# Kernel tuning notes

Hardware: AMD Instinct MI355X
Metric: run time of the kernel (lower is better)

Reference implementation:

```python
import jax, jax.numpy as jnp
import numpy as np

NUM_HEADS = 16
HEAD_DIM = 64  # hidden = 1024


def setup_inputs() -> dict:
    key = jax.random.key(0)
    k1, k2, k3 = jax.random.split(key, 3)
    B, S, Hd = 4, 4096, NUM_HEADS * HEAD_DIM
    x = jax.random.normal(k1, (B, S, Hd), dtype=jnp.float32)
    # xavier-uniform-ish scaling for the dense kernels
    Wqkv = jax.random.normal(k2, (Hd, 3 * Hd), dtype=jnp.float32) * (2.0 / (Hd + 3 * Hd)) ** 0.5
    bqkv = jnp.zeros((3 * Hd,), dtype=jnp.float32)
    Wout = jax.random.normal(k3, (Hd, Hd), dtype=jnp.float32) * (1.0 / Hd) ** 0.5
    bout = jnp.zeros((Hd,), dtype=jnp.float32)
    return {"x": x, "Wqkv": Wqkv, "bqkv": bqkv, "Wout": Wout, "bout": bout}


def reference(x, Wqkv, bqkv, Wout, bout):
    B, S, _ = x.shape
    H, D = NUM_HEADS, HEAD_DIM
    qkv = jnp.einsum('bsc,cf->bsf', x, Wqkv) + bqkv  # [B,S,3*H*D]
    q, k, v = jnp.split(qkv, 3, axis=-1)
    # source transposes to [B,H,S,D] before calling flax dot_product_attention_weights,
    # which interprets dims as [..., q_len=H, num_heads=S, depth=D]  (shape bug, kept faithfully)
    q = q.reshape(B, S, H, D).transpose(0, 2, 1, 3)  # [B,H,S,D]
    k = k.reshape(B, S, H, D).transpose(0, 2, 1, 3)
    v = v.reshape(B, S, H, D).transpose(0, 2, 1, 3)
    scale = D ** -0.5
    # flax: einsum('...qhd,...khd->...hqk') -> weights [B, S, H, H]
    logits = jnp.einsum('bqhd,bkhd->bhqk', q * scale, k)
    attn = jax.nn.softmax(logits, axis=-1)  # softmax over key-head axis
    # source: einsum('bhqk,bkhd->bqhd', weights, v) -> [B, H, S, D]
    out = jnp.einsum('bhqk,bkhd->bqhd', attn, v)
    out = out.transpose(0, 2, 1, 3).reshape(B, S, H * D)  # [B,S,hidden]
    return jnp.einsum('bsc,cf->bsf', out, Wout) + bout
```

## Files before the change

kernel.cpp:

```cpp
#include <hip/hip_runtime.h>
#include <hip/hip_bf16.h>

using bf16 = __hip_bfloat16;
typedef __bf16 bf16x8_t __attribute__((ext_vector_type(8)));
typedef float f32x4_t __attribute__((ext_vector_type(4)));

__device__ __forceinline__ void gl16(bf16* l, const bf16* g) {
  __builtin_amdgcn_global_load_lds(
      (const __attribute__((address_space(1))) unsigned int*)g,
      (__attribute__((address_space(3))) unsigned int*)l, 16, 0, 0);
}

__global__ __launch_bounds__(256) void cvt_f32_bf16(const float* __restrict__ in,
                                                    bf16* __restrict__ out, int n4) {
  int i = blockIdx.x * 256 + threadIdx.x;
  if (i >= n4) return;
  float4 v = ((const float4*)in)[i];
  union { ushort4 u; bf16 b[4]; } o;
  o.b[0] = __float2bfloat16(v.x);
  o.b[1] = __float2bfloat16(v.y);
  o.b[2] = __float2bfloat16(v.z);
  o.b[3] = __float2bfloat16(v.w);
  ((ushort4*)out)[i] = o.u;
}

__global__ __launch_bounds__(256) void transpose_cvt(const float* __restrict__ in,
                                                     bf16* __restrict__ out, int R, int C) {
  __shared__ float t[32][33];
  int bx = blockIdx.x * 32, by = blockIdx.y * 32;
  int tx = threadIdx.x & 31, ty = threadIdx.x >> 5;
#pragma unroll
  for (int r = 0; r < 32; r += 8)
    t[ty + r][tx] = in[(size_t)(by + ty + r) * C + bx + tx];
  __syncthreads();
#pragma unroll
  for (int r = 0; r < 32; r += 8)
    out[(size_t)(bx + ty + r) * R + by + tx] = __float2bfloat16(t[tx][ty + r]);
}

template <int OUT_BF16>
__global__ __launch_bounds__(256, 2) void gemm_bt(const bf16* __restrict__ A,
                                                  const bf16* __restrict__ Bt,
                                                  const float* __restrict__ bias,
                                                  void* __restrict__ Cv,
                                                  int M, int N, int K) {
  __shared__ __align__(16) bf16 As[128 * 32];
  __shared__ __align__(16) bf16 Bs[128 * 32];
  const int tid = threadIdx.x;
  const int m0 = blockIdx.y * 128, n0 = blockIdx.x * 128;
  const int w = tid >> 6, lane = tid & 63;
  const int wr = w >> 1, wc = w & 1;
  const int lr = lane & 15, lk = (lane >> 4) << 3;

  const int srow = tid >> 2;
  const int scol = (tid & 3) << 3;
  const bf16* ga0 = A + (size_t)(m0 + srow) * K + scol;
  const bf16* ga1 = A + (size_t)(m0 + srow + 64) * K + scol;
  const bf16* gb0 = Bt + (size_t)(n0 + srow) * K + scol;
  const bf16* gb1 = Bt + (size_t)(n0 + srow + 64) * K + scol;
  bf16* la0 = As + tid * 8;
  bf16* la1 = As + (tid + 256) * 8;
  bf16* lb0 = Bs + tid * 8;
  bf16* lb1 = Bs + (tid + 256) * 8;

  f32x4_t acc[4][4] = {};

  for (int k0 = 0; k0 < K; k0 += 32) {
    gl16(la0, ga0); gl16(la1, ga1);
    gl16(lb0, gb0); gl16(lb1, gb1);
    ga0 += 32; ga1 += 32; gb0 += 32; gb1 += 32;
    __syncthreads();

    bf16x8_t af[4], bfv[4];
#pragma unroll
    for (int m = 0; m < 4; ++m)
      af[m] = *(const bf16x8_t*)(As + ((wr * 64 + m * 16 + lr) * 32 + lk));
#pragma unroll
    for (int n = 0; n < 4; ++n)
      bfv[n] = *(const bf16x8_t*)(Bs + ((wc * 64 + n * 16 + lr) * 32 + lk));
#pragma unroll
    for (int m = 0; m < 4; ++m)
#pragma unroll
      for (int n = 0; n < 4; ++n)
        acc[m][n] = __builtin_amdgcn_mfma_f32_16x16x32_bf16(af[m], bfv[n], acc[m][n], 0, 0, 0);
    __syncthreads();
  }

  const int r0 = (lane >> 4) << 2;
#pragma unroll
  for (int m = 0; m < 4; ++m) {
    int row = m0 + wr * 64 + m * 16 + r0;
#pragma unroll
    for (int n = 0; n < 4; ++n) {
      int col = n0 + wc * 64 + n * 16 + lr;
      float bv = bias[col];
#pragma unroll
      for (int j = 0; j < 4; ++j) {
        float v = acc[m][n][j] + bv;
        if (OUT_BF16)
          ((bf16*)Cv)[(size_t)(row + j) * N + col] = __float2bfloat16(v);
        else
          ((float*)Cv)[(size_t)(row + j) * N + col] = v;
      }
    }
  }
}

#define PSTR 48
__global__ __launch_bounds__(256) void attn_tok(const bf16* __restrict__ qkv,
                                                bf16* __restrict__ out) {
  __shared__ __align__(16) bf16 vs[4][1024];
  __shared__ __align__(16) bf16 ps[4][16 * PSTR];
  const int w = threadIdx.x >> 6, l = threadIdx.x & 63;
  const int t = blockIdx.x * 4 + w;
  const int lr = l & 15, lg = l >> 4;
  const bf16* base = qkv + (size_t)t * 3072;

  bf16x8_t v0 = *(const bf16x8_t*)(base + 2048 + l * 16);
  bf16x8_t v1 = *(const bf16x8_t*)(base + 2048 + l * 16 + 8);
  *(bf16x8_t*)(&vs[w][l * 16]) = v0;
  *(bf16x8_t*)(&vs[w][l * 16 + 8]) = v1;

  *(unsigned long long*)(&ps[w][(l >> 2) * PSTR + 16 + (l & 3) * 4]) = 0ULL;

  const bf16* qp = base + lr * 64 + lg * 8;
  const bf16* kp = base + 1024 + lr * 64 + lg * 8;
  bf16x8_t qa0 = *(const bf16x8_t*)qp;
  bf16x8_t ka0 = *(const bf16x8_t*)kp;
  bf16x8_t qa1 = *(const bf16x8_t*)(qp + 32);
  bf16x8_t ka1 = *(const bf16x8_t*)(kp + 32);
  f32x4_t s = {};
  s = __builtin_amdgcn_mfma_f32_16x16x32_bf16(qa0, ka0, s, 0, 0, 0);
  s = __builtin_amdgcn_mfma_f32_16x16x32_bf16(qa1, ka1, s, 0, 0, 0);

#pragma unroll
  for (int j = 0; j < 4; ++j) {
    float x = s[j] * 0.125f;
    float mx = x;
#pragma unroll
    for (int off = 8; off; off >>= 1) mx = fmaxf(mx, __shfl_xor(mx, off, 16));
    float e = __expf(x - mx);
    float sum = e;
#pragma unroll
    for (int off = 8; off; off >>= 1) sum += __shfl_xor(sum, off, 16);
    ps[w][(lg * 4 + j) * PSTR + lr] = __float2bfloat16(e / sum);
  }

  bf16x8_t pf = *(const bf16x8_t*)(&ps[w][lr * PSTR + lg * 8]);
  bf16x8_t vf[4] = {};
  if (l < 32) {
#pragma unroll
    for (int c = 0; c < 4; ++c)
#pragma unroll
      for (int j = 0; j < 8; ++j)
        vf[c][j] = (__bf16)vs[w][(lg * 8 + j) * 64 + c * 16 + lr];
  }
  f32x4_t o[4] = {};
#pragma unroll
  for (int c = 0; c < 4; ++c)
    o[c] = __builtin_amdgcn_mfma_f32_16x16x32_bf16(pf, vf[c], o[c], 0, 0, 0);

  bf16* ob = out + (size_t)t * 1024;
#pragma unroll
  for (int c = 0; c < 4; ++c)
#pragma unroll
    for (int j = 0; j < 4; ++j)
      ob[(lg * 4 + j) * 64 + c * 16 + lr] = __float2bfloat16(o[c][j]);
}

extern "C" void kernel_launch(void* const* d_in, const int* in_sizes, int n_in,
                              void* d_out, int out_size, void* d_ws, size_t ws_size,
                              hipStream_t stream) {
  const float* x    = (const float*)d_in[0];
  const float* Wqkv = (const float*)d_in[1];
  const float* bqkv = (const float*)d_in[2];
  const float* Wout = (const float*)d_in[3];
  const float* bout = (const float*)d_in[4];
  float* y = (float*)d_out;

  const int T = 16384, HD = 1024, N1 = 3072;

  char* ws = (char*)d_ws;
  size_t off = 0;
  bf16* xb  = (bf16*)(ws + off); off += (size_t)T * HD * 2;
  bf16* w1t = (bf16*)(ws + off); off += (size_t)N1 * HD * 2;
  bf16* w2t = (bf16*)(ws + off); off += (size_t)HD * HD * 2;
  bf16* qkv = (bf16*)(ws + off); off += (size_t)T * N1 * 2;
  if (ws_size < off) return;
  bf16* ao = xb;

  cvt_f32_bf16<<<(T * HD / 4 + 255) / 256, 256, 0, stream>>>(x, xb, T * HD / 4);
  transpose_cvt<<<dim3(N1 / 32, HD / 32), 256, 0, stream>>>(Wqkv, w1t, HD, N1);
  transpose_cvt<<<dim3(HD / 32, HD / 32), 256, 0, stream>>>(Wout, w2t, HD, HD);

  gemm_bt<1><<<dim3(N1 / 128, T / 128), 256, 0, stream>>>(xb, w1t, bqkv, qkv, T, N1, HD);
  attn_tok<<<T / 4, 256, 0, stream>>>(qkv, ao);
  gemm_bt<0><<<dim3(HD / 128, T / 128), 256, 0, stream>>>(ao, w2t, bout, y, T, HD, HD);
}
```

Measured before the change: 232.2 us.

## Replace 128x128 GEMM with pipelined 256x256 tile kernel using swizzled LDS

New measurement: 220.1 us. 1.05x faster.

```diff
diff --git a/kernel.cpp b/kernel.cpp
--- a/kernel.cpp
+++ b/kernel.cpp
@@ -10,6 +10,9 @@
       (const __attribute__((address_space(1))) unsigned int*)g,
       (__attribute__((address_space(3))) unsigned int*)l, 16, 0, 0);
 }
+
+#define BARRIER() do { asm volatile("" ::: "memory"); __builtin_amdgcn_s_barrier(); asm volatile("" ::: "memory"); } while (0)
+#define WAITVM(N) asm volatile("s_waitcnt vmcnt(" #N ")" ::: "memory")
 
 __global__ __launch_bounds__(256) void cvt_f32_bf16(const float* __restrict__ in,
                                                     bf16* __restrict__ out, int n4) {
@@ -38,62 +41,124 @@
     out[(size_t)(bx + ty + r) * R + by + tx] = __float2bfloat16(t[tx][ty + r]);
 }
 
+
+template <int MH, int NH>
+__device__ __forceinline__ void phase_loads(const bf16* lb, int wr, int wc, int lr, int lg, int exr,
+                                            bf16x8_t (&af)[4][2], bf16x8_t (&bfr)[2][2]) {
+  const bf16* ab = lb + MH * 8192;
+  const bf16* bb = lb + (2 + NH) * 8192;
+#pragma unroll
+  for (int mi = 0; mi < 4; ++mi) {
+    int R = wr * 64 + mi * 16 + lr;
+    af[mi][0] = *(const bf16x8_t*)(ab + R * 64 + ((lg * 8) ^ exr));
+    af[mi][1] = *(const bf16x8_t*)(ab + R * 64 + ((32 + lg * 8) ^ exr));
+  }
+#pragma unroll
+  for (int ni = 0; ni < 2; ++ni) {
+    int R = wc * 32 + ni * 16 + lr;
+    bfr[ni][0] = *(const bf16x8_t*)(bb + R * 64 + ((lg * 8) ^ exr));
+    bfr[ni][1] = *(const bf16x8_t*)(bb + R * 64 + ((32 + lg * 8) ^ exr));
+  }
+}
+
+template <int MH, int NH>
+__device__ __forceinline__ void phase_mfma(bf16x8_t (&af)[4][2], bf16x8_t (&bfr)[2][2],
+                                           f32x4_t (&acc)[8][4]) {
+  __builtin_amdgcn_s_setprio(1);
+#pragma unroll
+  for (int mi = 0; mi < 4; ++mi)
+#pragma unroll
+    for (int ni = 0; ni < 2; ++ni) {
+      f32x4_t& a = acc[MH * 4 + mi][NH * 2 + ni];
+      a = __builtin_amdgcn_mfma_f32_16x16x32_bf16(af[mi][0], bfr[ni][0], a, 0, 0, 0);
+      a = __builtin_amdgcn_mfma_f32_16x16x32_bf16(af[mi][1], bfr[ni][1], a, 0, 0, 0);
+    }
+  __builtin_amdgcn_s_setprio(0);
+}
+
+#define DO_PHASE(BUF, MH, NH, STAGE, WAIT) do {                          \
+    bf16x8_t af[4][2], bfr[2][2];                                        \
+    phase_loads<MH, NH>(lds + (BUF) * 32768, wr, wc, lr, lg, exr, af, bfr); \
+    STAGE; WAIT;                                                         \
+    BARRIER();                                                           \
+    phase_mfma<MH, NH>(af, bfr, acc);                                    \
+    BARRIER();                                                           \
+  } while (0)
+
 template <int OUT_BF16>
-__global__ __launch_bounds__(256, 2) void gemm_bt(const bf16* __restrict__ A,
+__global__ __launch_bounds__(512, 2) void gemm256(const bf16* __restrict__ A,
                                                   const bf16* __restrict__ Bt,
                                                   const float* __restrict__ bias,
                                                   void* __restrict__ Cv,
                                                   int M, int N, int K) {
-  __shared__ __align__(16) bf16 As[128 * 32];
-  __shared__ __align__(16) bf16 Bs[128 * 32];
+  __shared__ __align__(16) bf16 lds[65536];
   const int tid = threadIdx.x;
-  const int m0 = blockIdx.y * 128, n0 = blockIdx.x * 128;
-  const int w = tid >> 6, lane = tid & 63;
-  const int wr = w >> 1, wc = w & 1;
-  const int lr = lane & 15, lk = (lane >> 4) << 3;
-
-  const int srow = tid >> 2;
-  const int scol = (tid & 3) << 3;
-  const bf16* ga0 = A + (size_t)(m0 + srow) * K + scol;
-  const bf16* ga1 = A + (size_t)(m0 + srow + 64) * K + scol;
-  const bf16* gb0 = Bt + (size_t)(n0 + srow) * K + scol;
-  const bf16* gb1 = Bt + (size_t)(n0 + srow + 64) * K + scol;
-  bf16* la0 = As + tid * 8;
-  bf16* la1 = As + (tid + 256) * 8;
-  bf16* lb0 = Bs + tid * 8;
-  bf16* lb1 = Bs + (tid + 256) * 8;
-
-  f32x4_t acc[4][4] = {};
-
-  for (int k0 = 0; k0 < K; k0 += 32) {
-    gl16(la0, ga0); gl16(la1, ga1);
-    gl16(lb0, gb0); gl16(lb1, gb1);
-    ga0 += 32; ga1 += 32; gb0 += 32; gb1 += 32;
-    __syncthreads();
-
-    bf16x8_t af[4], bfv[4];
-#pragma unroll
-    for (int m = 0; m < 4; ++m)
-      af[m] = *(const bf16x8_t*)(As + ((wr * 64 + m * 16 + lr) * 32 + lk));
-#pragma unroll
-    for (int n = 0; n < 4; ++n)
-      bfv[n] = *(const bf16x8_t*)(Bs + ((wc * 64 + n * 16 + lr) * 32 + lk));
-#pragma unroll
-    for (int m = 0; m < 4; ++m)
-#pragma unroll
-      for (int n = 0; n < 4; ++n)
-        acc[m][n] = __builtin_amdgcn_mfma_f32_16x16x32_bf16(af[m], bfv[n], acc[m][n], 0, 0, 0);
-    __syncthreads();
-  }
-
-  const int r0 = (lane >> 4) << 2;
-#pragma unroll
-  for (int m = 0; m < 4; ++m) {
-    int row = m0 + wr * 64 + m * 16 + r0;
-#pragma unroll
-    for (int n = 0; n < 4; ++n) {
-      int col = n0 + wc * 64 + n * 16 + lr;
-      float bv = bias[col];
+  const int nwgx = gridDim.x;
+  int orig = blockIdx.y * nwgx + blockIdx.x;
+  int cpx = (nwgx * gridDim.y) >> 3;
+  int swzid = (orig & 7) * cpx + (orig >> 3);
+  const int m0 = (swzid / nwgx) * 256, n0 = (swzid % nwgx) * 256;
+
+  const int wid = tid >> 6, lane = tid & 63;
+  const int wr = wid >> 2, wc = wid & 3;
+  const int lr = lane & 15, lg = lane >> 4;
+  const int exr = (lr & 7) << 3;
+
+  const int srow = tid >> 3;
+  const int colg = ((((tid & 7) * 16) ^ ((srow & 7) << 4)) >> 1);
+  const int browc0 = (srow >> 5) * 64 + (srow & 31);
+
+  auto stageA = [&](int b2, int h, int kt) {
+    const bf16* g0 = A + (size_t)(m0 + h * 64 + srow) * K + kt * 64 + colg;
+    const bf16* g1 = A + (size_t)(m0 + 128 + h * 64 + srow) * K + kt * 64 + colg;
+    bf16* l = lds + b2 * 32768 + h * 8192 + tid * 8;
+    gl16(l, g0); gl16(l + 4096, g1);
+  };
+  auto stageB = [&](int b2, int h, int kt) {
+    const bf16* g0 = Bt + (size_t)(n0 + browc0 + h * 32) * K + kt * 64 + colg;
+    const bf16* g1 = Bt + (size_t)(n0 + 128 + browc0 + h * 32) * K + kt * 64 + colg;
+    bf16* l = lds + b2 * 32768 + (2 + h) * 8192 + tid * 8;
+    gl16(l, g0); gl16(l + 4096, g1);
+  };
+
+  f32x4_t acc[8][4] = {};
+  const int nt = K >> 6;
+
+  stageA(0, 0, 0); stageB(0, 0, 0); stageA(0, 1, 0); stageB(0, 1, 0);
+  stageA(1, 0, 1); stageB(1, 0, 1);
+  WAITVM(4);
+  BARRIER();
+
+  for (int t = 0; t <= nt - 3; ++t) {
+    const int buf = t & 1, bufn = buf ^ 1;
+    DO_PHASE(buf, 0, 0, stageA(bufn, 1, t + 1), (void)0);
+    DO_PHASE(buf, 0, 1, stageB(bufn, 1, t + 1), (void)0);
+    DO_PHASE(buf, 1, 0, stageA(buf, 0, t + 2), (void)0);
+    DO_PHASE(buf, 1, 1, stageB(buf, 0, t + 2), WAITVM(4));
+  }
+  {
+    const int t = nt - 2;
+    const int buf = t & 1, bufn = buf ^ 1;
+    DO_PHASE(buf, 0, 0, stageA(bufn, 1, t + 1), (void)0);
+    DO_PHASE(buf, 0, 1, stageB(bufn, 1, t + 1), (void)0);
+    DO_PHASE(buf, 1, 0, (void)0, (void)0);
+    DO_PHASE(buf, 1, 1, (void)0, WAITVM(0));
+  }
+  {
+    const int buf = (nt - 1) & 1;
+    DO_PHASE(buf, 0, 0, (void)0, (void)0);
+    DO_PHASE(buf, 0, 1, (void)0, (void)0);
+    DO_PHASE(buf, 1, 0, (void)0, (void)0);
+    DO_PHASE(buf, 1, 1, (void)0, (void)0);
+  }
+
+#pragma unroll
+  for (int n = 0; n < 4; ++n) {
+    int col = n0 + wc * 64 + n * 16 + lr;
+    float bv = bias[col];
+#pragma unroll
+    for (int m = 0; m < 8; ++m) {
+      int row = m0 + wr * 128 + m * 16 + lg * 4;
 #pragma unroll
       for (int j = 0; j < 4; ++j) {
         float v = acc[m][n][j] + bv;
@@ -193,7 +258,7 @@
   transpose_cvt<<<dim3(N1 / 32, HD / 32), 256, 0, stream>>>(Wqkv, w1t, HD, N1);
   transpose_cvt<<<dim3(HD / 32, HD / 32), 256, 0, stream>>>(Wout, w2t, HD, HD);
 
-  gemm_bt<1><<<dim3(N1 / 128, T / 128), 256, 0, stream>>>(xb, w1t, bqkv, qkv, T, N1, HD);
+  gemm256<1><<<dim3(N1 / 256, T / 256), 512, 0, stream>>>(xb, w1t, bqkv, qkv, T, N1, HD);
   attn_tok<<<T / 4, 256, 0, stream>>>(qkv, ao);
-  gemm_bt<0><<<dim3(HD / 128, T / 128), 256, 0, stream>>>(ao, w2t, bout, y, T, HD, HD);
-}
+  gemm256<0><<<dim3(HD / 256, T / 256), 512, 0, stream>>>(ao, w2t, bout, y, T, HD, HD);
+}
```
